# Optimization experiments

Hardware: AMD Instinct MI355X
Metric: run time of the kernel (lower is better)

The kernel has to match this reference:

```python
import jax, jax.numpy as jnp
import numpy as np

B, S, H, L = 64, 512, 768, 9


def setup_inputs() -> dict:
    key = jax.random.key(0)
    ks = jax.random.split(key, 8)
    hidden = jax.random.normal(ks[0], (B, S, H), jnp.float32)
    lengths = jax.random.randint(ks[1], (B,), S // 2, S + 1)
    attention_mask = (jnp.arange(S)[None, :] < lengths[:, None]).astype(jnp.int32)
    labels = jax.random.randint(ks[2], (B, S), 0, L)
    # sprinkle some -100 ignore labels like HF datasets do
    ignore = jax.random.uniform(ks[3], (B, S)) < 0.05
    labels = jnp.where(ignore, -100, labels)
    W = jax.random.normal(ks[4], (H, L), jnp.float32) * 0.02
    b = jnp.zeros((L,), jnp.float32)
    start_transitions = jax.random.uniform(ks[5], (L,), jnp.float32, -0.1, 0.1)
    end_transitions = jax.random.uniform(ks[6], (L,), jnp.float32, -0.1, 0.1)
    transitions = jax.random.uniform(ks[7], (L, L), jnp.float32, -0.1, 0.1)
    return dict(hidden=hidden, attention_mask=attention_mask, labels=labels, W=W, b=b,
                start_transitions=start_transitions, end_transitions=end_transitions,
                transitions=transitions)


def _crf_numerator(emissions, tags, maskf, start_t, end_t, trans):
    # score of the gold tag sequence (torchcrf _compute_score)
    first = start_t[tags[:, 0]] + jnp.take_along_axis(emissions[:, 0], tags[:, 0:1], axis=1)[:, 0]
    em = jnp.take_along_axis(emissions, tags[..., None], axis=2)[..., 0]      # [B,S]
    tr = trans[tags[:, :-1], tags[:, 1:]]                                     # [B,S-1]
    score = first + jnp.sum((em[:, 1:] + tr) * maskf[:, 1:], axis=1)
    last_idx = (jnp.sum(maskf, axis=1).astype(jnp.int32) - 1)
    last_tags = jnp.take_along_axis(tags, last_idx[:, None], axis=1)[:, 0]
    return score + end_t[last_tags]


def _crf_lognorm(emissions, maskf, start_t, end_t, trans):
    # forward algorithm (torchcrf _compute_normalizer) as a lax.scan
    score0 = start_t[None, :] + emissions[:, 0]                               # [B,L]
    em_seq = jnp.transpose(emissions[:, 1:], (1, 0, 2))                       # [S-1,B,L]
    m_seq = maskf[:, 1:].T                                                    # [S-1,B]

    def step(score, xs):
        em_t, m_t = xs
        nxt = jax.nn.logsumexp(score[:, :, None] + trans[None] + em_t[:, None, :], axis=1)
        return jnp.where(m_t[:, None] > 0, nxt, score), None

    score, _ = jax.lax.scan(step, score0, (em_seq, m_seq))
    return jax.nn.logsumexp(score + end_t[None, :], axis=1)


def _viterbi(emissions, maskf, start_t, end_t, trans):
    score0 = start_t[None, :] + emissions[:, 0]                               # [B,L]
    em_seq = jnp.transpose(emissions[:, 1:], (1, 0, 2))
    m_seq = maskf[:, 1:].T

    def step(score, xs):
        em_t, m_t = xs
        cand = score[:, :, None] + trans[None]                                # [B,L,L]
        bp = jnp.argmax(cand, axis=1)                                         # [B,L]
        nxt = jnp.max(cand, axis=1) + em_t
        return jnp.where(m_t[:, None] > 0, nxt, score), bp

    score, history = jax.lax.scan(step, score0, (em_seq, m_seq))              # history [S-1,B,L]
    best_last = jnp.argmax(score + end_t[None, :], axis=1)                    # [B]

    def back(cur, xs):
        bp_t, m_t = xs
        prev = jnp.where(m_t > 0, jnp.take_along_axis(bp_t, cur[:, None], axis=1)[:, 0], cur)
        return prev, prev

    _, tags_rev = jax.lax.scan(back, best_last, (history[::-1], m_seq[::-1]))
    tags = jnp.concatenate([tags_rev[::-1].T, best_last[:, None]], axis=1)    # [B,S]
    return tags


def reference(hidden, attention_mask, labels, W, b, start_transitions, end_transitions, transitions):
    maskf = attention_mask.astype(hidden.dtype)                               # [B,S]
    logits = jnp.einsum('bsh,hl->bsl', hidden, W) + b                         # [B,S,L]
    safe_labels = jnp.where(labels == -100, 0, labels)
    num = _crf_numerator(logits, safe_labels, maskf, start_transitions, end_transitions, transitions)
    den = _crf_lognorm(logits, maskf, start_transitions, end_transitions, transitions)
    loss = -jnp.mean(num - den)                                               # -crf(..., reduction='mean')
    tags = _viterbi(logits, maskf, start_transitions, end_transitions, transitions)
    fake_logits = jax.nn.one_hot(tags, L, dtype=logits.dtype) * maskf[..., None]
    return loss, fake_logits
```

## Files before the change

kernel.cpp:

```cpp
#include <hip/hip_runtime.h>
#include <hip/hip_bf16.h>
#include <stdint.h>

constexpr int BB  = 64;
constexpr int SS  = 512;
constexpr int HH  = 768;
constexpr int NL  = 9;
constexpr int NROWS = BB * SS;
constexpr int EMN   = SS * NL;
constexpr int NSEG  = 8;
constexpr float NEG  = -1e30f;

__device__ __forceinline__ float readlane_f(float v, int lane) {
  union { float f; int i; } u;
  u.f = v;
  u.i = __builtin_amdgcn_readlane(u.i, lane);
  return u.f;
}

__global__ __launch_bounds__(256, 2) void logits_kernel(
    const float* __restrict__ hidden, const float* __restrict__ W,
    const float* __restrict__ bias, const int* __restrict__ mask,
    float* __restrict__ logits, int* __restrict__ lens) {
  const int lane = threadIdx.x & 63;
  const int wid  = blockIdx.x * 4 + (threadIdx.x >> 6);

  if (blockIdx.x < 64 && threadIdx.x < 64) {
    const int4* mp = (const int4*)(mask + blockIdx.x * SS);
    const int4 a = mp[threadIdx.x];
    const int4 c = mp[threadIdx.x + 64];
    int lsum = a.x + a.y + a.z + a.w + c.x + c.y + c.z + c.w;
#pragma unroll
    for (int off = 32; off >= 1; off >>= 1) lsum += __shfl_xor(lsum, off, 64);
    if (threadIdx.x == 0) lens[blockIdx.x] = lsum;
  }

  float w[3][4][NL];
#pragma unroll
  for (int j = 0; j < 3; ++j)
#pragma unroll
    for (int k = 0; k < 4; ++k) {
      const int r = lane * 4 + j * 256 + k;
#pragma unroll
      for (int l = 0; l < NL; ++l) w[j][k][l] = W[r * NL + l];
    }
  const float my_bias = (lane < NL) ? bias[lane] : 0.0f;

#pragma unroll
  for (int rep = 0; rep < 2; ++rep) {
    const int rA = wid + rep * 16384;
    const int rB = rA + 8192;
    const float4* hA = (const float4*)(hidden + (size_t)rA * HH);
    const float4* hB = (const float4*)(hidden + (size_t)rB * HH);
    float accA[NL], accB[NL];
#pragma unroll
    for (int l = 0; l < NL; ++l) { accA[l] = 0.0f; accB[l] = 0.0f; }
#pragma unroll
    for (int j = 0; j < 3; ++j) {
      const float4 a = hA[lane + j * 64];
      const float4 b = hB[lane + j * 64];
#pragma unroll
      for (int l = 0; l < NL; ++l) {
        accA[l] += a.x * w[j][0][l] + a.y * w[j][1][l] +
                   a.z * w[j][2][l] + a.w * w[j][3][l];
        accB[l] += b.x * w[j][0][l] + b.y * w[j][1][l] +
                   b.z * w[j][2][l] + b.w * w[j][3][l];
      }
    }
#pragma unroll
    for (int off = 32; off >= 1; off >>= 1)
#pragma unroll
      for (int l = 0; l < NL; ++l) {
        accA[l] += __shfl_xor(accA[l], off, 64);
        accB[l] += __shfl_xor(accB[l], off, 64);
      }
    if (lane < NL) {
      float vA = accA[0], vB = accB[0];
#pragma unroll
      for (int l = 1; l < NL; ++l)
        if (lane == l) { vA = accA[l]; vB = accB[l]; }
      logits[(size_t)rA * NL + lane] = vA + my_bias;
      logits[(size_t)rB * NL + lane] = vB + my_bias;
    }
  }
}

__global__ __launch_bounds__(64) void scan_kernel(
    const float* __restrict__ logits, const int* __restrict__ labels,
    const float* __restrict__ start_t, const float* __restrict__ end_t,
    const float* __restrict__ trans, float* __restrict__ out,
    float* __restrict__ num_den, const int* __restrict__ lens,
    float* __restrict__ segmat) {
  __shared__ unsigned char bp_s[EMN + 80];
  __shared__ unsigned char tags_s[SS];
  __shared__ int lab[SS];

  const int blk = blockIdx.x;
  const int tid = threadIdx.x;
  const int j   = (tid < NL) ? tid : NL - 1;

  if (blk < 64) {
    const int b   = blk;
    const int len = lens[b];
    const float* emb = logits + (size_t)b * EMN;
    float tc[NL];
#pragma unroll
    for (int i = 0; i < NL; ++i) tc[i] = trans[i * NL + j];
    float s[NL];
#pragma unroll
    for (int i = 0; i < NL; ++i) s[i] = start_t[i] + emb[i];
    float eA = emb[1 * NL + j], eB = emb[2 * NL + j];
    float eC = emb[3 * NL + j], eD = emb[4 * NL + j];
    for (int t = 1; t < len; ++t) {
      float c[NL];
#pragma unroll
      for (int i = 0; i < NL; ++i) c[i] = s[i] + tc[i];
      const float x01 = fmaxf(c[0], c[1]), x23 = fmaxf(c[2], c[3]);
      const float x45 = fmaxf(c[4], c[5]), x67 = fmaxf(c[6], c[7]);
      const float best = fmaxf(fmaxf(fmaxf(x01, x23), fmaxf(x45, x67)), c[8]);
      const float nxt = best + eA;
      {
        const bool b01 = c[0] >= c[1], b23 = c[2] >= c[3];
        const bool b45 = c[4] >= c[5], b67 = c[6] >= c[7];
        const float v01 = b01 ? c[0] : c[1]; const int i01 = b01 ? 0 : 1;
        const float v23 = b23 ? c[2] : c[3]; const int i23 = b23 ? 2 : 3;
        const float v45 = b45 ? c[4] : c[5]; const int i45 = b45 ? 4 : 5;
        const float v67 = b67 ? c[6] : c[7]; const int i67 = b67 ? 6 : 7;
        const bool bA = v01 >= v23, bB = v45 >= v67;
        const float vA = bA ? v01 : v23; const int iA = bA ? i01 : i23;
        const float vB = bB ? v45 : v67; const int iB = bB ? i45 : i67;
        const bool bC = vA >= vB;
        const float vC = bC ? vA : vB; const int iC = bC ? iA : iB;
        const bool bD = vC >= c[8];
        const int arg = bD ? iC : 8;
        bp_s[t * NL + tid] = (unsigned char)arg;
      }
#pragma unroll
      for (int i = 0; i < NL; ++i) s[i] = readlane_f(nxt, i);
      eA = eB; eB = eC; eC = eD;
      eD = emb[(t + 4) * NL + j];
    }
    float bv = s[0] + end_t[0];
    int   bl = 0;
#pragma unroll
    for (int i = 1; i < NL; ++i) {
      const float cc = s[i] + end_t[i];
      if (cc > bv) { bv = cc; bl = i; }
    }
    __syncthreads();

    uint64_t C = 0x876543210ULL;
#pragma unroll
    for (int k = 1; k <= 8; ++k) {
      const int t = 8 * tid + k;
      uint64_t nc = 0;
#pragma unroll
      for (int x = 0; x < 9; ++x) {
        const int g = bp_s[t * NL + x] & 15;
        nc |= ((C >> (4 * g)) & 15ULL) << (4 * x);
      }
      C = (t < len) ? nc : C;
    }
    const uint32_t Clo = (uint32_t)C, Chi = (uint32_t)(C >> 32);
    uint32_t cur = (uint32_t)bl;
    int bnd = 0;
#pragma unroll
    for (int c = 63; c >= 0; --c) {
      bnd = (tid == c) ? (int)cur : bnd;
      const uint32_t lo = (uint32_t)__builtin_amdgcn_readlane((int)Clo, c);
      const uint32_t hi = (uint32_t)__builtin_amdgcn_readlane((int)Chi, c);
      const uint64_t cc = ((uint64_t)hi << 32) | lo;
      cur = (uint32_t)((cc >> (4 * cur)) & 15u);
    }
    int tag = bnd;
#pragma unroll
    for (int k = 8; k >= 1; --k) {
      const int t = 8 * tid + k;
      const int tt = (t < 512) ? t : 511;
      const int nt = bp_s[tt * NL + tag];
      tag = (t < len) ? nt : tag;
      tags_s[t - 1] = (unsigned char)tag;
    }
    __syncthreads();
    for (int i = tid; i < EMN; i += 64) {
      const int t = i / NL;
      const int l = i - t * NL;
      out[1 + (size_t)b * EMN + i] =
          (t < len && l == (int)tags_s[t]) ? 1.0f : 0.0f;
    }

  } else if (blk < 128) {
    const int b   = blk - 64;
    const int len = lens[b];
    const float* emb = logits + (size_t)b * EMN;
    for (int t = tid; t < SS; t += 64) {
      const int v = labels[b * SS + t];
      lab[t] = (v == -100) ? 0 : v;
    }
    __syncthreads();
    float contrib = 0.0f;
    for (int t = tid; t < SS; t += 64) {
      if (t >= 1 && t < len)
        contrib += emb[t * NL + lab[t]] + trans[lab[t - 1] * NL + lab[t]];
    }
#pragma unroll
    for (int off = 32; off >= 1; off >>= 1)
      contrib += __shfl_xor(contrib, off, 64);
    if (tid == 0) {
      const int l0 = lab[0];
      num_den[b] = start_t[l0] + emb[l0] + contrib + end_t[lab[len - 1]];
    }

  } else {
    const int id  = blk - 128;
    const int b   = id / 72;
    const int rem = id - b * 72;
    const int sg  = rem / 9;
    const int e   = rem - sg * 9;
    const int len = lens[b];
    const float* emb = logits + (size_t)b * EMN;
    float tc[NL];
#pragma unroll
    for (int i = 0; i < NL; ++i) tc[i] = trans[i * NL + j];
    float s[NL];
#pragma unroll
    for (int i = 0; i < NL; ++i) s[i] = (i == e) ? 0.0f : NEG;
    float my = (j == e) ? 0.0f : NEG;
    const int tbeg = 64 * sg + 1;
    const int tlast = (64 * sg + 64 < 511) ? 64 * sg + 64 : 511;
    float eA = emb[tbeg * NL + j],       eB = emb[(tbeg + 1) * NL + j];
    float eC = emb[(tbeg + 2) * NL + j], eD = emb[(tbeg + 3) * NL + j];
    for (int t = tbeg; t <= tlast; ++t) {
      if (t >= len) break;
      float c[NL];
#pragma unroll
      for (int i = 0; i < NL; ++i) c[i] = s[i] + tc[i];
      const float x01 = fmaxf(c[0], c[1]), x23 = fmaxf(c[2], c[3]);
      const float x45 = fmaxf(c[4], c[5]), x67 = fmaxf(c[6], c[7]);
      const float m = fmaxf(fmaxf(fmaxf(x01, x23), fmaxf(x45, x67)), c[8]);
      float sum = 0.0f;
#pragma unroll
      for (int i = 0; i < NL; ++i) sum += __expf(c[i] - m);
      const float nxt = m + __logf(sum) + eA;
      my = nxt;
#pragma unroll
      for (int i = 0; i < NL; ++i) s[i] = readlane_f(nxt, i);
      eA = eB; eB = eC; eC = eD;
      eD = emb[(t + 4) * NL + j];
    }
    if (tid < NL)
      segmat[((size_t)(b * NSEG + sg) * NL + e) * NL + tid] = my;
  }
}

__global__ __launch_bounds__(64) void combine_kernel(
    const float* __restrict__ logits, const float* __restrict__ segmat,
    const float* __restrict__ start_t, const float* __restrict__ end_t,
    float* __restrict__ num_den) {
  const int b   = blockIdx.x;
  const int tid = threadIdx.x;
  const int j   = (tid < NL) ? tid : NL - 1;
  float s[NL];
#pragma unroll
  for (int i = 0; i < NL; ++i) s[i] = start_t[i] + logits[(size_t)b * EMN + i];
  float mcur[NL], mnxt[NL];
  {
    const float* M = segmat + (size_t)(b * NSEG) * 81;
#pragma unroll
    for (int i = 0; i < NL; ++i) mcur[i] = M[i * NL + j];
  }
  for (int sg = 0; sg < NSEG; ++sg) {
    if (sg + 1 < NSEG) {
      const float* M = segmat + (size_t)(b * NSEG + sg + 1) * 81;
#pragma unroll
      for (int i = 0; i < NL; ++i) mnxt[i] = M[i * NL + j];
    }
    float c[NL];
#pragma unroll
    for (int i = 0; i < NL; ++i) c[i] = s[i] + mcur[i];
    const float x01 = fmaxf(c[0], c[1]), x23 = fmaxf(c[2], c[3]);
    const float x45 = fmaxf(c[4], c[5]), x67 = fmaxf(c[6], c[7]);
    const float m = fmaxf(fmaxf(fmaxf(x01, x23), fmaxf(x45, x67)), c[8]);
    float sum = 0.0f;
#pragma unroll
    for (int i = 0; i < NL; ++i) sum += __expf(c[i] - m);
    const float nxt = m + __logf(sum);
#pragma unroll
    for (int i = 0; i < NL; ++i) s[i] = readlane_f(nxt, i);
#pragma unroll
    for (int i = 0; i < NL; ++i) mcur[i] = mnxt[i];
  }
  float c[NL];
#pragma unroll
  for (int i = 0; i < NL; ++i) c[i] = s[i] + end_t[i];
  const float x01 = fmaxf(c[0], c[1]), x23 = fmaxf(c[2], c[3]);
  const float x45 = fmaxf(c[4], c[5]), x67 = fmaxf(c[6], c[7]);
  const float m = fmaxf(fmaxf(fmaxf(x01, x23), fmaxf(x45, x67)), c[8]);
  float sum = 0.0f;
#pragma unroll
  for (int i = 0; i < NL; ++i) sum += __expf(c[i] - m);
  if (tid == 0) num_den[64 + b] = m + __logf(sum);
}

__global__ __launch_bounds__(64) void loss_kernel(
    const float* __restrict__ num_den, float* __restrict__ out) {
  const int tid = threadIdx.x;
  float v = num_den[64 + tid] - num_den[tid];
#pragma unroll
  for (int off = 32; off >= 1; off >>= 1) v += __shfl_xor(v, off, 64);
  if (tid == 0) out[0] = v * (1.0f / 64.0f);
}

extern "C" void kernel_launch(void* const* d_in, const int* in_sizes, int n_in,
                              void* d_out, int out_size, void* d_ws, size_t ws_size,
                              hipStream_t stream) {
  const float* hidden  = (const float*)d_in[0];
  const int*   mask    = (const int*)d_in[1];
  const int*   labels  = (const int*)d_in[2];
  const float* W       = (const float*)d_in[3];
  const float* bias    = (const float*)d_in[4];
  const float* start_t = (const float*)d_in[5];
  const float* end_t   = (const float*)d_in[6];
  const float* trans   = (const float*)d_in[7];
  float* out = (float*)d_out;

  float* logits  = (float*)d_ws;
  float* segmat  = logits + (size_t)NROWS * NL;
  float* num_den = segmat + (size_t)BB * NSEG * 81;
  int*   lens    = (int*)(num_den + 128);

  logits_kernel<<<2048, 256, 0, stream>>>(hidden, W, bias, mask, logits, lens);
  scan_kernel<<<4736, 64, 0, stream>>>(logits, labels, start_t, end_t, trans,
                                       out, num_den, lens, segmat);
  combine_kernel<<<64, 64, 0, stream>>>(logits, segmat, start_t, end_t, num_den);
  loss_kernel<<<1, 64, 0, stream>>>(num_den, out);
}
```

Before: 259.5 us.

## Batch three CRF start states per wave, hoist hidden loads, fold loss into combine

Each scan wavefront now carries three independent start-state recurrences for a segment instead of one. This gives the serial logsumexp chain more instruction-level parallelism and cuts the segment-scan grid from 4736 to 1664 blocks. The logits kernel issues all four rows' hidden loads up front before computing, which raises memory-level parallelism. The separate loss kernel is removed; the combine kernel atomically accumulates into a memset output, saving one launch at the cost of a memset and nondeterministic float summation order.

```diff
diff --git a/kernel.cpp b/kernel.cpp
--- a/kernel.cpp
+++ b/kernel.cpp
@@ -46,41 +46,40 @@
     }
   const float my_bias = (lane < NL) ? bias[lane] : 0.0f;
 
-#pragma unroll
-  for (int rep = 0; rep < 2; ++rep) {
-    const int rA = wid + rep * 16384;
-    const int rB = rA + 8192;
-    const float4* hA = (const float4*)(hidden + (size_t)rA * HH);
-    const float4* hB = (const float4*)(hidden + (size_t)rB * HH);
-    float accA[NL], accB[NL];
-#pragma unroll
-    for (int l = 0; l < NL; ++l) { accA[l] = 0.0f; accB[l] = 0.0f; }
-#pragma unroll
-    for (int j = 0; j < 3; ++j) {
-      const float4 a = hA[lane + j * 64];
-      const float4 b = hB[lane + j * 64];
-#pragma unroll
-      for (int l = 0; l < NL; ++l) {
-        accA[l] += a.x * w[j][0][l] + a.y * w[j][1][l] +
-                   a.z * w[j][2][l] + a.w * w[j][3][l];
-        accB[l] += b.x * w[j][0][l] + b.y * w[j][1][l] +
-                   b.z * w[j][2][l] + b.w * w[j][3][l];
-      }
-    }
-#pragma unroll
-    for (int off = 32; off >= 1; off >>= 1)
-#pragma unroll
-      for (int l = 0; l < NL; ++l) {
-        accA[l] += __shfl_xor(accA[l], off, 64);
-        accB[l] += __shfl_xor(accB[l], off, 64);
-      }
-    if (lane < NL) {
-      float vA = accA[0], vB = accB[0];
-#pragma unroll
-      for (int l = 1; l < NL; ++l)
-        if (lane == l) { vA = accA[l]; vB = accB[l]; }
-      logits[(size_t)rA * NL + lane] = vA + my_bias;
-      logits[(size_t)rB * NL + lane] = vB + my_bias;
+  float4 h[4][3];
+#pragma unroll
+  for (int r = 0; r < 4; ++r) {
+    const float4* hp = (const float4*)(hidden + (size_t)(wid + r * 8192) * HH);
+#pragma unroll
+    for (int j = 0; j < 3; ++j) h[r][j] = hp[lane + j * 64];
+  }
+  float acc[4][NL];
+#pragma unroll
+  for (int r = 0; r < 4; ++r)
+#pragma unroll
+    for (int l = 0; l < NL; ++l) acc[r][l] = 0.0f;
+#pragma unroll
+  for (int r = 0; r < 4; ++r)
+#pragma unroll
+    for (int j = 0; j < 3; ++j)
+#pragma unroll
+      for (int l = 0; l < NL; ++l)
+        acc[r][l] += h[r][j].x * w[j][0][l] + h[r][j].y * w[j][1][l] +
+                     h[r][j].z * w[j][2][l] + h[r][j].w * w[j][3][l];
+#pragma unroll
+  for (int off = 32; off >= 1; off >>= 1)
+#pragma unroll
+    for (int r = 0; r < 4; ++r)
+#pragma unroll
+      for (int l = 0; l < NL; ++l)
+        acc[r][l] += __shfl_xor(acc[r][l], off, 64);
+  if (lane < NL) {
+#pragma unroll
+    for (int r = 0; r < 4; ++r) {
+      float v = acc[r][0];
+#pragma unroll
+      for (int l = 1; l < NL; ++l) if (lane == l) v = acc[r][l];
+      logits[(size_t)(wid + r * 8192) * NL + lane] = v + my_bias;
     }
   }
 }
@@ -212,51 +211,78 @@
     }
 
   } else {
-    const int id  = blk - 128;
-    const int b   = id / 72;
-    const int rem = id - b * 72;
-    const int sg  = rem / 9;
-    const int e   = rem - sg * 9;
-    const int len = lens[b];
+    const int id   = blk - 128;
+    const int pair = id / 3;
+    const int wv   = id - pair * 3;
+    const int b    = pair >> 3;
+    const int sg   = pair & 7;
+    const int e0   = 3 * wv;
+    const int len  = lens[b];
     const float* emb = logits + (size_t)b * EMN;
     float tc[NL];
 #pragma unroll
     for (int i = 0; i < NL; ++i) tc[i] = trans[i * NL + j];
-    float s[NL];
-#pragma unroll
-    for (int i = 0; i < NL; ++i) s[i] = (i == e) ? 0.0f : NEG;
-    float my = (j == e) ? 0.0f : NEG;
-    const int tbeg = 64 * sg + 1;
+    float s0[NL], s1[NL], s2[NL];
+#pragma unroll
+    for (int i = 0; i < NL; ++i) {
+      s0[i] = (i == e0)     ? 0.0f : NEG;
+      s1[i] = (i == e0 + 1) ? 0.0f : NEG;
+      s2[i] = (i == e0 + 2) ? 0.0f : NEG;
+    }
+    float my0 = (j == e0)     ? 0.0f : NEG;
+    float my1 = (j == e0 + 1) ? 0.0f : NEG;
+    float my2 = (j == e0 + 2) ? 0.0f : NEG;
+    const int tbeg  = 64 * sg + 1;
     const int tlast = (64 * sg + 64 < 511) ? 64 * sg + 64 : 511;
     float eA = emb[tbeg * NL + j],       eB = emb[(tbeg + 1) * NL + j];
     float eC = emb[(tbeg + 2) * NL + j], eD = emb[(tbeg + 3) * NL + j];
     for (int t = tbeg; t <= tlast; ++t) {
       if (t >= len) break;
-      float c[NL];
-#pragma unroll
-      for (int i = 0; i < NL; ++i) c[i] = s[i] + tc[i];
-      const float x01 = fmaxf(c[0], c[1]), x23 = fmaxf(c[2], c[3]);
-      const float x45 = fmaxf(c[4], c[5]), x67 = fmaxf(c[6], c[7]);
-      const float m = fmaxf(fmaxf(fmaxf(x01, x23), fmaxf(x45, x67)), c[8]);
-      float sum = 0.0f;
-#pragma unroll
-      for (int i = 0; i < NL; ++i) sum += __expf(c[i] - m);
-      const float nxt = m + __logf(sum) + eA;
-      my = nxt;
-#pragma unroll
-      for (int i = 0; i < NL; ++i) s[i] = readlane_f(nxt, i);
+      float c0[NL], c1[NL], c2[NL];
+#pragma unroll
+      for (int i = 0; i < NL; ++i) {
+        c0[i] = s0[i] + tc[i];
+        c1[i] = s1[i] + tc[i];
+        c2[i] = s2[i] + tc[i];
+      }
+      const float m0 = fmaxf(fmaxf(fmaxf(fmaxf(c0[0], c0[1]), fmaxf(c0[2], c0[3])),
+                                   fmaxf(fmaxf(c0[4], c0[5]), fmaxf(c0[6], c0[7]))), c0[8]);
+      const float m1 = fmaxf(fmaxf(fmaxf(fmaxf(c1[0], c1[1]), fmaxf(c1[2], c1[3])),
+                                   fmaxf(fmaxf(c1[4], c1[5]), fmaxf(c1[6], c1[7]))), c1[8]);
+      const float m2 = fmaxf(fmaxf(fmaxf(fmaxf(c2[0], c2[1]), fmaxf(c2[2], c2[3])),
+                                   fmaxf(fmaxf(c2[4], c2[5]), fmaxf(c2[6], c2[7]))), c2[8]);
+      float u0 = 0.0f, u1 = 0.0f, u2 = 0.0f;
+#pragma unroll
+      for (int i = 0; i < NL; ++i) {
+        u0 += __expf(c0[i] - m0);
+        u1 += __expf(c1[i] - m1);
+        u2 += __expf(c2[i] - m2);
+      }
+      my0 = m0 + __logf(u0) + eA;
+      my1 = m1 + __logf(u1) + eA;
+      my2 = m2 + __logf(u2) + eA;
+#pragma unroll
+      for (int i = 0; i < NL; ++i) {
+        s0[i] = readlane_f(my0, i);
+        s1[i] = readlane_f(my1, i);
+        s2[i] = readlane_f(my2, i);
+      }
       eA = eB; eB = eC; eC = eD;
       eD = emb[(t + 4) * NL + j];
     }
-    if (tid < NL)
-      segmat[((size_t)(b * NSEG + sg) * NL + e) * NL + tid] = my;
+    if (tid < NL) {
+      float* M = segmat + (size_t)(b * NSEG + sg) * 81;
+      M[(e0    ) * NL + tid] = my0;
+      M[(e0 + 1) * NL + tid] = my1;
+      M[(e0 + 2) * NL + tid] = my2;
+    }
   }
 }
 
 __global__ __launch_bounds__(64) void combine_kernel(
     const float* __restrict__ logits, const float* __restrict__ segmat,
     const float* __restrict__ start_t, const float* __restrict__ end_t,
-    float* __restrict__ num_den) {
+    const float* __restrict__ num_den, float* __restrict__ out) {
   const int b   = blockIdx.x;
   const int tid = threadIdx.x;
   const int j   = (tid < NL) ? tid : NL - 1;
@@ -299,16 +325,10 @@
   float sum = 0.0f;
 #pragma unroll
   for (int i = 0; i < NL; ++i) sum += __expf(c[i] - m);
-  if (tid == 0) num_den[64 + b] = m + __logf(sum);
-}
-
-__global__ __launch_bounds__(64) void loss_kernel(
-    const float* __restrict__ num_den, float* __restrict__ out) {
-  const int tid = threadIdx.x;
-  float v = num_den[64 + tid] - num_den[tid];
-#pragma unroll
-  for (int off = 32; off >= 1; off >>= 1) v += __shfl_xor(v, off, 64);
-  if (tid == 0) out[0] = v * (1.0f / 64.0f);
+  if (tid == 0) {
+    const float den = m + __logf(sum);
+    atomicAdd(out, (den - num_den[b]) * (1.0f / 64.0f));
+  }
 }
 
 extern "C" void kernel_launch(void* const* d_in, const int* in_sizes, int n_in,
@@ -329,9 +349,10 @@
   float* num_den = segmat + (size_t)BB * NSEG * 81;
   int*   lens    = (int*)(num_den + 128);
 
+  hipMemsetAsync(out, 0, sizeof(float), stream);
   logits_kernel<<<2048, 256, 0, stream>>>(hidden, W, bias, mask, logits, lens);
-  scan_kernel<<<4736, 64, 0, stream>>>(logits, labels, start_t, end_t, trans,
+  scan_kernel<<<1664, 64, 0, stream>>>(logits, labels, start_t, end_t, trans,
                                        out, num_den, lens, segmat);
-  combine_kernel<<<64, 64, 0, stream>>>(logits, segmat, start_t, end_t, num_den);
-  loss_kernel<<<1, 64, 0, stream>>>(num_den, out);
-}
+  combine_kernel<<<64, 64, 0, stream>>>(logits, segmat, start_t, end_t,
+                                        num_den, out);
+}
```

After: 258.5 us. No clear change (-0.4%).
